# Optimization experiments

Hardware: AMD Instinct MI355X
Metric: run time of the kernel (lower is better)

Reference implementation:

```python
import jax, jax.numpy as jnp
import numpy as np

TOP_K = 2  # config.moe_config['moe_top_k']


def setup_inputs() -> dict:
    key = jax.random.key(0)
    k1, k2, k3, k4 = jax.random.split(key, 4)
    B, S, H, F, E = 2, 1024, 1024, 2048, 8
    def init(k, shape, fan_in):
        return jax.random.normal(k, shape, jnp.float32) / np.float32(np.sqrt(fan_in))
    return {
        "hidden_states": jax.random.normal(k1, (B, S, H), jnp.float32),
        "router_w": init(k2, (H, E), H),          # Linear(hidden, E, bias=False)
        "W1": init(k3, (E, H, 2 * F), H),          # per-expert Linear(hidden, 2*ffn)
        "W2": init(k4, (E, F, H), F),              # per-expert Linear(ffn, hidden)
    }


def reference(hidden_states, router_w, W1, W2):
    B, S, H = hidden_states.shape
    E = router_w.shape[1]
    x = hidden_states.reshape(-1, H)                      # [N, H], N = B*S
    N = x.shape[0]

    # router: logits -> fp32 softmax -> top-k -> renormalize (matches torch)
    logits = x @ router_w                                  # [N, E]
    probs = jax.nn.softmax(logits.astype(jnp.float32), axis=-1)
    rw, sel = jax.lax.top_k(probs, TOP_K)                  # [N, k]
    rw = rw / rw.sum(axis=-1, keepdims=True)
    rw = rw.astype(x.dtype)

    # combine weights per (token, expert); top-k experts are distinct so add==set
    cw = jnp.zeros((N, E), x.dtype).at[jnp.arange(N)[:, None], sel].add(rw)

    # per-expert SwiGLU MLP over all tokens, masked combine (full-capacity MoE)
    h = jnp.einsum('nh,ehf->enf', x, W1)                   # [E, N, 2F]
    a, b = jnp.split(h, 2, axis=-1)                        # gate, value halves
    g = jax.nn.silu(a) * b                                 # [E, N, F]
    y = jnp.einsum('enf,efh->enh', g, W2)                  # [E, N, H]
    out = jnp.einsum('enh,ne->nh', y, cw)                  # weighted scatter-combine
    return out.reshape(B, S, H)
```

## Files before the change

kernel.cpp:

```cpp
#include <hip/hip_runtime.h>
#include <hip/hip_bf16.h>

#define H_DIM 1024
#define E_NUM 8
#define F_DIM 2048
#define N_TOK 2048
typedef unsigned int uint;
typedef short bf16x8 __attribute__((ext_vector_type(8)));
typedef float f32x4 __attribute__((ext_vector_type(4)));

#define WS_CNT   0
#define WS_LIST  256
#define WS_W     (WS_LIST + 8*N_TOK*4)
#define WS_G     131072
#define WS_Y     (WS_G + 4096*2048*2)
#define WS_XB    WS_Y


static __device__ __forceinline__ uint f2bf(float f) {
    uint u = __builtin_bit_cast(uint, f);
    return (u + 0x7FFFu + ((u >> 16) & 1u)) >> 16;
}
static __device__ __forceinline__ float bflo(uint u) { return __builtin_bit_cast(float, u << 16); }
static __device__ __forceinline__ float bfhi(uint u) { return __builtin_bit_cast(float, u & 0xFFFF0000u); }
static __device__ __forceinline__ uint cvtpk(float a, float b) {
    uint r;
    asm("v_cvt_pk_bf16_f32 %0, %1, %2" : "=v"(r) : "v"(a), "v"(b));
    return r;
}
static __device__ __forceinline__ void gload_lds16(const void* g, void* l) {
    __builtin_amdgcn_global_load_lds(
        (const __attribute__((address_space(1))) unsigned int*)g,
        (__attribute__((address_space(3))) unsigned int*)l,
        16, 0, 0);
}
template<int N> static __device__ __forceinline__ void vmwait() {
    if constexpr (N == 0)       asm volatile("s_waitcnt vmcnt(0)" ::: "memory");
    else if constexpr (N == 10) asm volatile("s_waitcnt vmcnt(10)" ::: "memory");
}

__global__ __launch_bounds__(256) void cvt_x_kernel(const float* __restrict__ x,
                                                    unsigned short* __restrict__ xb)
{
    int c = blockIdx.x * 256 + threadIdx.x;
    int row = c >> 7, b = c & 127;
    int t = b >> 3, s = b & 7;
    int klo = t*64 + (s >> 2)*32 + (s & 3)*4;
    const float* xr = x + (size_t)row * H_DIM;
    float4 lo = *(const float4*)(xr + klo);
    float4 hi = *(const float4*)(xr + klo + 16);
    uint4 o;
    o.x = cvtpk(lo.x, lo.y); o.y = cvtpk(lo.z, lo.w);
    o.z = cvtpk(hi.x, hi.y); o.w = cvtpk(hi.z, hi.w);
    *(uint4*)(xb + (size_t)row * H_DIM + b*8) = o;
}

__global__ __launch_bounds__(256) void router_kernel(
    const float* __restrict__ x, const float* __restrict__ rw,
    int* __restrict__ cnt, int* __restrict__ list, float* __restrict__ w_entry)
{
    int wave = threadIdx.x >> 6, lane = threadIdx.x & 63;
    int n = blockIdx.x * 4 + wave;
    const float* xr = x + (size_t)n * H_DIM;
    float acc[8] = {0,0,0,0,0,0,0,0};
    #pragma unroll
    for (int i = 0; i < H_DIM/64; ++i) {
        int h = i*64 + lane;
        float xv = xr[h];
        const float4* rr = (const float4*)(rw + (size_t)h*8);
        float4 r0 = rr[0], r1 = rr[1];
        acc[0] += xv*r0.x; acc[1] += xv*r0.y; acc[2] += xv*r0.z; acc[3] += xv*r0.w;
        acc[4] += xv*r1.x; acc[5] += xv*r1.y; acc[6] += xv*r1.z; acc[7] += xv*r1.w;
    }
    #pragma unroll
    for (int e = 0; e < 8; ++e) {
        float v = acc[e];
        #pragma unroll
        for (int off = 32; off; off >>= 1) v += __shfl_xor(v, off);
        acc[e] = v;
    }
    int e0 = 0;
    #pragma unroll
    for (int e = 1; e < 8; ++e) if (acc[e] > acc[e0]) e0 = e;
    int e1 = -1;
    #pragma unroll
    for (int e = 0; e < 8; ++e) if (e != e0 && (e1 < 0 || acc[e] > acc[e1])) e1 = e;
    float w0 = 1.0f / (1.0f + __expf(acc[e1] - acc[e0]));
    float w1 = 1.0f - w0;
    if (lane == 0) {
        int p0 = atomicAdd(&cnt[e0], 1);
        list[e0*N_TOK + p0] = n*2;
        w_entry[n*2] = w0;
        int p1 = atomicAdd(&cnt[e1], 1);
        list[e1*N_TOK + p1] = n*2 + 1;
        w_entry[n*2+1] = w1;
    }
}

template<int IS_G1>
__global__ __launch_bounds__(256, 2) void moe_gemm_kernel(
    const unsigned short* __restrict__ Asrc, const float* __restrict__ W,
    const int* __restrict__ cnt, const int* __restrict__ list,
    const float* __restrict__ w_entry, unsigned short* __restrict__ dst)
{
    constexpr int KTOT  = IS_G1 ? H_DIM : F_DIM;
    constexpr int BLD   = IS_G1 ? 2*F_DIM : H_DIM;
    constexpr int DLD   = IS_G1 ? F_DIM : H_DIM;
    constexpr int ALD   = IS_G1 ? H_DIM : F_DIM;
    constexpr int NMT   = 32;
    constexpr int NNT   = IS_G1 ? 32 : 8;
    constexpr int NT    = KTOT / 64;

    __shared__ __align__(16) unsigned short As[2][64*64];
    __shared__ __align__(16) uint Bs[2][64*128];

    constexpr int nb = NMT * NNT * E_NUM;
    constexpr int chunk = nb >> 3;
    int bid = blockIdx.x;
    int f  = (bid & 7) * chunk + (bid >> 3);
    int mt = f % NMT;
    int nt = (f / NMT) % NNT;
    int e  = f / (NMT * NNT);

    const int c = cnt[e];
    if (mt * 64 >= c) return;
    const int tid = threadIdx.x;
    const int lane = tid & 63, wid = tid >> 6;
    const int l15 = lane & 15, lg = lane >> 4;
    const int lbase = e * N_TOK + mt * 64;

    const unsigned short* a_src[2];
    #pragma unroll
    for (int i = 0; i < 2; ++i) {
        int sl  = wid*2048 + i*1024 + lane*16;
        int row = sl >> 7;
        int kb  = ((sl >> 4) & 7) ^ (row & 7);
        int rr  = (mt*64 + row) < c ? row : (c - 1 - mt*64);
        int ent = list[lbase + rr];
        int arow = IS_G1 ? (ent >> 1) : ent;
        a_src[i] = Asrc + (size_t)arow * ALD + kb*8;
    }

    const float* Wb = W + (size_t)e * (size_t)(IS_G1 ? H_DIM*2*F_DIM : F_DIM*H_DIM);
    const float* b_srcp[8];
    #pragma unroll
    for (int i = 0; i < 8; ++i) {
        int k  = wid*16 + i*2 + (lane >> 5);
        int c4 = (lane & 31) ^ (k & 12);
        int gc;
        if constexpr (IS_G1) gc = (c4 < 16) ? (nt*64 + 4*c4) : (F_DIM + nt*64 + 4*(c4-16));
        else                 gc = nt*128 + 4*c4;
        b_srcp[i] = Wb + (size_t)k * BLD + gc;
    }

    int a_addr[4][2];
    #pragma unroll
    for (int m = 0; m < 4; ++m)
        #pragma unroll
        for (int kk = 0; kk < 2; ++kk) {
            int row = m*16 + l15;
            a_addr[m][kk] = row*128 + ((kk*64 + lg*16) ^ ((row & 7) << 4));
        }
    int b_base[2];
    #pragma unroll
    for (int j = 0; j < 2; ++j) {
        int cb = j ? (4 + wid) : wid;
        b_base[j] = ((cb*16 + l15) * 4) ^ (lg << 6);
    }

    f32x4 acc[4][2];
    #pragma unroll
    for (int m = 0; m < 4; ++m)
        #pragma unroll
        for (int j = 0; j < 2; ++j) acc[m][j] = (f32x4){0.f,0.f,0.f,0.f};

    auto STAGE = [&](int tt) {
        const int b = tt & 1;
        #pragma unroll
        for (int i = 0; i < 2; ++i)
            gload_lds16(a_src[i] + tt*64, (char*)As[b] + wid*2048 + i*1024);
        #pragma unroll
        for (int i = 0; i < 8; ++i)
            gload_lds16(b_srcp[i] + (size_t)tt * 64 * BLD, (char*)Bs[b] + wid*8192 + i*1024);
    };

    auto compute_step = [&](const char* ab, const char* bb0) {
        #pragma unroll
        for (int kk = 0; kk < 2; ++kk) {
            bf16x8 af[4];
            #pragma unroll
            for (int m = 0; m < 4; ++m)
                af[m] = *(const bf16x8*)(ab + a_addr[m][kk]);
            bf16x8 bfr[2];
            #pragma unroll
            for (int j = 0; j < 2; ++j) {
                const char* bb = bb0 + (kk*32 + 4*lg)*512 + b_base[j];
                float fA0 = *(const float*)(bb);
                float fA1 = *(const float*)(bb + 512);
                float fA2 = *(const float*)(bb + 1024);
                float fA3 = *(const float*)(bb + 1536);
                float fB0 = *(const float*)(bb + 8192);
                float fB1 = *(const float*)(bb + 8192 + 512);
                float fB2 = *(const float*)(bb + 8192 + 1024);
                float fB3 = *(const float*)(bb + 8192 + 1536);
                union { uint u[4]; bf16x8 v; } bu;
                bu.u[0] = cvtpk(fA0, fA1);
                bu.u[1] = cvtpk(fA2, fA3);
                bu.u[2] = cvtpk(fB0, fB1);
                bu.u[3] = cvtpk(fB2, fB3);
                bfr[j] = bu.v;
            }
            #pragma unroll
            for (int m = 0; m < 4; ++m)
                #pragma unroll
                for (int j = 0; j < 2; ++j)
                    acc[m][j] = __builtin_amdgcn_mfma_f32_16x16x32_bf16(af[m], bfr[j], acc[m][j], 0, 0, 0);
        }
    };

    STAGE(0);
    STAGE(1);

    #pragma unroll
    for (int t = 0; t < NT; ++t) {
        if (t < NT - 1) vmwait<10>();
        else            vmwait<0>();
        __builtin_amdgcn_sched_barrier(0);
        __builtin_amdgcn_s_barrier();
        asm volatile("" ::: "memory");
        compute_step((const char*)As[t & 1], (const char*)Bs[t & 1]);
        if (t + 2 < NT) {
            asm volatile("" ::: "memory");
            __builtin_amdgcn_s_barrier();
            asm volatile("" ::: "memory");
            STAGE(t + 2);
        }
    }

    if constexpr (IS_G1) {
        const int pbase = nt*64 + ((wid >> 1)*4 + (l15 >> 2))*8 + (wid & 1)*4 + (l15 & 3);
        #pragma unroll
        for (int m = 0; m < 4; ++m) {
            f32x4 ga = acc[m][0], gv = acc[m][1];
            #pragma unroll
            for (int i = 0; i < 4; ++i) {
                int rl = m*16 + lg*4 + i;
                if (mt*64 + rl < c) {
                    int ent = list[lbase + rl];
                    float a = ga[i];
                    float g = (a / (1.f + __expf(-a))) * gv[i];
                    dst[(size_t)ent * DLD + pbase] = (unsigned short)f2bf(g);
                }
            }
        }
    } else {
        #pragma unroll
        for (int m = 0; m < 4; ++m)
            #pragma unroll
            for (int i = 0; i < 4; ++i) {
                int rl = m*16 + lg*4 + i;
                if (mt*64 + rl < c) {
                    int ent = list[lbase + rl];
                    float w = w_entry[ent];
                    #pragma unroll
                    for (int j = 0; j < 2; ++j) {
                        int col = nt*128 + (j ? (64 + wid*16) : (wid*16)) + l15;
                        dst[(size_t)ent * DLD + col] = (unsigned short)f2bf(w * acc[m][j][i]);
                    }
                }
            }
    }
}

__global__ __launch_bounds__(256) void combine_kernel(
    const unsigned short* __restrict__ y, float* __restrict__ out)
{
    int gid = blockIdx.x * 256 + threadIdx.x;
    size_t base = (size_t)gid * 8;
    int n = (int)(base >> 10), h = (int)(base & 1023);
    const uint4 a = *(const uint4*)(y + (size_t)(2*n)   * 1024 + h);
    const uint4 b = *(const uint4*)(y + (size_t)(2*n+1) * 1024 + h);
    float4 o0, o1;
    o0.x = bflo(a.x)+bflo(b.x); o0.y = bfhi(a.x)+bfhi(b.x);
    o0.z = bflo(a.y)+bflo(b.y); o0.w = bfhi(a.y)+bfhi(b.y);
    o1.x = bflo(a.z)+bflo(b.z); o1.y = bfhi(a.z)+bfhi(b.z);
    o1.z = bflo(a.w)+bflo(b.w); o1.w = bfhi(a.w)+bfhi(b.w);
    *(float4*)(out + base)     = o0;
    *(float4*)(out + base + 4) = o1;
}

extern "C" void kernel_launch(void* const* d_in, const int* in_sizes, int n_in,
                              void* d_out, int out_size, void* d_ws, size_t ws_size,
                              hipStream_t stream) {
    const float* x  = (const float*)d_in[0];
    const float* rw = (const float*)d_in[1];
    const float* W1 = (const float*)d_in[2];
    const float* W2 = (const float*)d_in[3];
    float* out = (float*)d_out;
    char* ws = (char*)d_ws;
    int*   cnt     = (int*)(ws + WS_CNT);
    int*   list    = (int*)(ws + WS_LIST);
    float* w_entry = (float*)(ws + WS_W);
    unsigned short* g  = (unsigned short*)(ws + WS_G);
    unsigned short* y  = (unsigned short*)(ws + WS_Y);
    unsigned short* xb = (unsigned short*)(ws + WS_XB);

    hipMemsetAsync(cnt, 0, E_NUM * sizeof(int), stream);
    cvt_x_kernel<<<N_TOK*H_DIM/2048, 256, 0, stream>>>(x, xb);
    router_kernel<<<N_TOK/4, 256, 0, stream>>>(x, rw, cnt, list, w_entry);
    moe_gemm_kernel<1><<<32*32*E_NUM, 256, 0, stream>>>(xb, W1, cnt, list, w_entry, g);
    moe_gemm_kernel<0><<<32*8*E_NUM, 256, 0, stream>>>(g,  W2, cnt, list, w_entry, y);
    combine_kernel<<<(out_size/8 + 255)/256, 256, 0, stream>>>(y, out);
}
```

Before: 254.2 us.

## Shrink K-step and GEMM2 row tile, raise occupancy, stage epilogue through LDS

The K step of the grouped GEMM pipeline drops from 64 to 32 so each B buffer is half the size. The A tile is staged once per two B stages. GEMM2 now uses 32-row tiles with twice as many blocks, and launch bounds ask for 3 or 4 blocks per CU instead of 2, which should improve occupancy and latency hiding. Both epilogues now transpose results through shared memory so each thread writes 16- or 32-byte vectors per gathered row instead of scattered 2-byte stores. In exchange there are more barriers per K, and GEMM2 blocks do less work each, so the W2 tile is re-read more often.

Result: faster. 237.4 us (-6.6%).

```diff
diff --git a/kernel.cpp b/kernel.cpp
--- a/kernel.cpp
+++ b/kernel.cpp
@@ -35,8 +35,10 @@
         16, 0, 0);
 }
 template<int N> static __device__ __forceinline__ void vmwait() {
-    if constexpr (N == 0)       asm volatile("s_waitcnt vmcnt(0)" ::: "memory");
-    else if constexpr (N == 10) asm volatile("s_waitcnt vmcnt(10)" ::: "memory");
+    if constexpr (N == 0)      asm volatile("s_waitcnt vmcnt(0)" ::: "memory");
+    else if constexpr (N == 4) asm volatile("s_waitcnt vmcnt(4)" ::: "memory");
+    else if constexpr (N == 5) asm volatile("s_waitcnt vmcnt(5)" ::: "memory");
+    else if constexpr (N == 6) asm volatile("s_waitcnt vmcnt(6)" ::: "memory");
 }
 
 __global__ __launch_bounds__(256) void cvt_x_kernel(const float* __restrict__ x,
@@ -98,7 +100,7 @@
 }
 
 template<int IS_G1>
-__global__ __launch_bounds__(256, 2) void moe_gemm_kernel(
+__global__ __launch_bounds__(256, IS_G1 ? 3 : 4) void moe_gemm_kernel(
     const unsigned short* __restrict__ Asrc, const float* __restrict__ W,
     const int* __restrict__ cnt, const int* __restrict__ list,
     const float* __restrict__ w_entry, unsigned short* __restrict__ dst)
@@ -107,12 +109,16 @@
     constexpr int BLD   = IS_G1 ? 2*F_DIM : H_DIM;
     constexpr int DLD   = IS_G1 ? F_DIM : H_DIM;
     constexpr int ALD   = IS_G1 ? H_DIM : F_DIM;
-    constexpr int NMT   = 32;
+    constexpr int ROWS  = IS_G1 ? 64 : 32;
+    constexpr int NM    = ROWS / 16;
+    constexpr int NA    = ROWS / 32;
+    constexpr int NMT   = 2048 / ROWS;
     constexpr int NNT   = IS_G1 ? 32 : 8;
-    constexpr int NT    = KTOT / 64;
-
-    __shared__ __align__(16) unsigned short As[2][64*64];
-    __shared__ __align__(16) uint Bs[2][64*128];
+    constexpr int NT    = KTOT / 32;
+    constexpr int ODDW  = 4 + NA;
+
+    __shared__ __align__(16) unsigned short As[2][ROWS*64];
+    __shared__ __align__(16) uint Bs[2][32*128];
 
     constexpr int nb = NMT * NNT * E_NUM;
     constexpr int chunk = nb >> 3;
@@ -123,29 +129,29 @@
     int e  = f / (NMT * NNT);
 
     const int c = cnt[e];
-    if (mt * 64 >= c) return;
+    if (mt * ROWS >= c) return;
     const int tid = threadIdx.x;
     const int lane = tid & 63, wid = tid >> 6;
     const int l15 = lane & 15, lg = lane >> 4;
-    const int lbase = e * N_TOK + mt * 64;
-
-    const unsigned short* a_src[2];
-    #pragma unroll
-    for (int i = 0; i < 2; ++i) {
-        int sl  = wid*2048 + i*1024 + lane*16;
+    const int lbase = e * N_TOK + mt * ROWS;
+
+    const unsigned short* a_src[NA];
+    #pragma unroll
+    for (int i = 0; i < NA; ++i) {
+        int sl  = wid*(NA*1024) + i*1024 + lane*16;
         int row = sl >> 7;
         int kb  = ((sl >> 4) & 7) ^ (row & 7);
-        int rr  = (mt*64 + row) < c ? row : (c - 1 - mt*64);
+        int rr  = (mt*ROWS + row) < c ? row : (c - 1 - mt*ROWS);
         int ent = list[lbase + rr];
         int arow = IS_G1 ? (ent >> 1) : ent;
         a_src[i] = Asrc + (size_t)arow * ALD + kb*8;
     }
 
     const float* Wb = W + (size_t)e * (size_t)(IS_G1 ? H_DIM*2*F_DIM : F_DIM*H_DIM);
-    const float* b_srcp[8];
-    #pragma unroll
-    for (int i = 0; i < 8; ++i) {
-        int k  = wid*16 + i*2 + (lane >> 5);
+    const float* b_srcp[4];
+    #pragma unroll
+    for (int i = 0; i < 4; ++i) {
+        int k  = wid*8 + i*2 + (lane >> 5);
         int c4 = (lane & 31) ^ (k & 12);
         int gc;
         if constexpr (IS_G1) gc = (c4 < 16) ? (nt*64 + 4*c4) : (F_DIM + nt*64 + 4*(c4-16));
@@ -153,122 +159,159 @@
         b_srcp[i] = Wb + (size_t)k * BLD + gc;
     }
 
-    int a_addr[4][2];
-    #pragma unroll
-    for (int m = 0; m < 4; ++m)
-        #pragma unroll
-        for (int kk = 0; kk < 2; ++kk) {
+    int a_addr[NM][2];
+    #pragma unroll
+    for (int m = 0; m < NM; ++m)
+        #pragma unroll
+        for (int p = 0; p < 2; ++p) {
             int row = m*16 + l15;
-            a_addr[m][kk] = row*128 + ((kk*64 + lg*16) ^ ((row & 7) << 4));
+            a_addr[m][p] = row*128 + ((p*64 + lg*16) ^ ((row & 7) << 4));
         }
     int b_base[2];
     #pragma unroll
     for (int j = 0; j < 2; ++j) {
-        int cb = j ? (4 + wid) : wid;
+        int cb = IS_G1 ? (j ? (4 + wid) : wid) : (wid*2 + j);
         b_base[j] = ((cb*16 + l15) * 4) ^ (lg << 6);
     }
 
-    f32x4 acc[4][2];
-    #pragma unroll
-    for (int m = 0; m < 4; ++m)
+    f32x4 acc[NM][2];
+    #pragma unroll
+    for (int m = 0; m < NM; ++m)
         #pragma unroll
         for (int j = 0; j < 2; ++j) acc[m][j] = (f32x4){0.f,0.f,0.f,0.f};
 
-    auto STAGE = [&](int tt) {
-        const int b = tt & 1;
-        #pragma unroll
-        for (int i = 0; i < 2; ++i)
-            gload_lds16(a_src[i] + tt*64, (char*)As[b] + wid*2048 + i*1024);
-        #pragma unroll
-        for (int i = 0; i < 8; ++i)
-            gload_lds16(b_srcp[i] + (size_t)tt * 64 * BLD, (char*)Bs[b] + wid*8192 + i*1024);
+    auto STAGE_A = [&](int s) {
+        #pragma unroll
+        for (int i = 0; i < NA; ++i)
+            gload_lds16(a_src[i] + s*64, (char*)As[s & 1] + wid*(NA*1024) + i*1024);
     };
-
-    auto compute_step = [&](const char* ab, const char* bb0) {
-        #pragma unroll
-        for (int kk = 0; kk < 2; ++kk) {
-            bf16x8 af[4];
+    auto STAGE_B = [&](int t) {
+        #pragma unroll
+        for (int i = 0; i < 4; ++i)
+            gload_lds16(b_srcp[i] + (size_t)t * 32 * BLD, (char*)Bs[t & 1] + wid*4096 + i*1024);
+    };
+    auto compute = [&](int P, int abuf) {
+        const char* ab  = (const char*)As[abuf];
+        const char* bb0 = (const char*)Bs[P];
+        bf16x8 af[NM];
+        #pragma unroll
+        for (int m = 0; m < NM; ++m)
+            af[m] = *(const bf16x8*)(ab + (P ? a_addr[m][1] : a_addr[m][0]));
+        bf16x8 bfr[2];
+        #pragma unroll
+        for (int j = 0; j < 2; ++j) {
+            const char* bb = bb0 + (4*lg)*512 + b_base[j];
+            float fA0 = *(const float*)(bb);
+            float fA1 = *(const float*)(bb + 512);
+            float fA2 = *(const float*)(bb + 1024);
+            float fA3 = *(const float*)(bb + 1536);
+            float fB0 = *(const float*)(bb + 8192);
+            float fB1 = *(const float*)(bb + 8192 + 512);
+            float fB2 = *(const float*)(bb + 8192 + 1024);
+            float fB3 = *(const float*)(bb + 8192 + 1536);
+            union { uint u[4]; bf16x8 v; } bu;
+            bu.u[0] = cvtpk(fA0, fA1);
+            bu.u[1] = cvtpk(fA2, fA3);
+            bu.u[2] = cvtpk(fB0, fB1);
+            bu.u[3] = cvtpk(fB2, fB3);
+            bfr[j] = bu.v;
+        }
+        #pragma unroll
+        for (int m = 0; m < NM; ++m)
             #pragma unroll
-            for (int m = 0; m < 4; ++m)
-                af[m] = *(const bf16x8*)(ab + a_addr[m][kk]);
-            bf16x8 bfr[2];
-            #pragma unroll
-            for (int j = 0; j < 2; ++j) {
-                const char* bb = bb0 + (kk*32 + 4*lg)*512 + b_base[j];
-                float fA0 = *(const float*)(bb);
-                float fA1 = *(const float*)(bb + 512);
-                float fA2 = *(const float*)(bb + 1024);
-                float fA3 = *(const float*)(bb + 1536);
-                float fB0 = *(const float*)(bb + 8192);
-                float fB1 = *(const float*)(bb + 8192 + 512);
-                float fB2 = *(const float*)(bb + 8192 + 1024);
-                float fB3 = *(const float*)(bb + 8192 + 1536);
-                union { uint u[4]; bf16x8 v; } bu;
-                bu.u[0] = cvtpk(fA0, fA1);
-                bu.u[1] = cvtpk(fA2, fA3);
-                bu.u[2] = cvtpk(fB0, fB1);
-                bu.u[3] = cvtpk(fB2, fB3);
-                bfr[j] = bu.v;
-            }
-            #pragma unroll
-            for (int m = 0; m < 4; ++m)
-                #pragma unroll
-                for (int j = 0; j < 2; ++j)
-                    acc[m][j] = __builtin_amdgcn_mfma_f32_16x16x32_bf16(af[m], bfr[j], acc[m][j], 0, 0, 0);
-        }
+            for (int j = 0; j < 2; ++j)
+                acc[m][j] = __builtin_amdgcn_mfma_f32_16x16x32_bf16(af[m], bfr[j], acc[m][j], 0, 0, 0);
     };
 
-    STAGE(0);
-    STAGE(1);
-
-    #pragma unroll
-    for (int t = 0; t < NT; ++t) {
-        if (t < NT - 1) vmwait<10>();
-        else            vmwait<0>();
+    STAGE_A(0); STAGE_B(0); STAGE_B(1);
+
+    for (int tp = 0; tp < NT/2 - 1; ++tp) {
+        const int t = 2*tp, ab = tp & 1;
+        vmwait<4>();
         __builtin_amdgcn_sched_barrier(0);
         __builtin_amdgcn_s_barrier();
         asm volatile("" ::: "memory");
-        compute_step((const char*)As[t & 1], (const char*)Bs[t & 1]);
-        if (t + 2 < NT) {
-            asm volatile("" ::: "memory");
-            __builtin_amdgcn_s_barrier();
-            asm volatile("" ::: "memory");
-            STAGE(t + 2);
-        }
+        compute(0, ab);
+        asm volatile("" ::: "memory");
+        __builtin_amdgcn_s_barrier();
+        asm volatile("" ::: "memory");
+        STAGE_A(tp + 1);
+        STAGE_B(t + 2);
+        vmwait<ODDW>();
+        __builtin_amdgcn_sched_barrier(0);
+        __builtin_amdgcn_s_barrier();
+        asm volatile("" ::: "memory");
+        compute(1, ab);
+        asm volatile("" ::: "memory");
+        __builtin_amdgcn_s_barrier();
+        asm volatile("" ::: "memory");
+        STAGE_B(t + 3);
+    }
+    {
+        const int ab = (NT/2 - 1) & 1;
+        vmwait<4>();
+        __builtin_amdgcn_sched_barrier(0);
+        __builtin_amdgcn_s_barrier();
+        asm volatile("" ::: "memory");
+        compute(0, ab);
+        asm volatile("" ::: "memory");
+        vmwait<0>();
+        __builtin_amdgcn_sched_barrier(0);
+        __builtin_amdgcn_s_barrier();
+        asm volatile("" ::: "memory");
+        compute(1, ab);
     }
 
     if constexpr (IS_G1) {
-        const int pbase = nt*64 + ((wid >> 1)*4 + (l15 >> 2))*8 + (wid & 1)*4 + (l15 & 3);
-        #pragma unroll
-        for (int m = 0; m < 4; ++m) {
+        unsigned short (*tb)[64] = (unsigned short (*)[64])As;
+        const int pcol = ((wid >> 1)*4 + (l15 >> 2))*8 + (wid & 1)*4 + (l15 & 3);
+        #pragma unroll
+        for (int m = 0; m < NM; ++m) {
             f32x4 ga = acc[m][0], gv = acc[m][1];
             #pragma unroll
             for (int i = 0; i < 4; ++i) {
-                int rl = m*16 + lg*4 + i;
-                if (mt*64 + rl < c) {
-                    int ent = list[lbase + rl];
-                    float a = ga[i];
-                    float g = (a / (1.f + __expf(-a))) * gv[i];
-                    dst[(size_t)ent * DLD + pbase] = (unsigned short)f2bf(g);
+                int row = m*16 + lg*4 + i;
+                float a = ga[i];
+                tb[row][pcol] = (unsigned short)f2bf((a / (1.f + __expf(-a))) * gv[i]);
+            }
+        }
+        __syncthreads();
+        int r = tid >> 3, ch = tid & 7;
+        #pragma unroll
+        for (int h = 0; h < 2; ++h) {
+            int rr = r + h*32;
+            if (mt*64 + rr < c) {
+                int ent = list[lbase + rr];
+                uint4 v = *(const uint4*)&tb[rr][ch*8];
+                *(uint4*)((char*)dst + ((size_t)ent * DLD + nt*64)*2 + ch*16) = v;
+            }
+        }
+    } else {
+        float (*tb)[128] = (float (*)[128])Bs;
+        #pragma unroll
+        for (int m = 0; m < NM; ++m)
+            #pragma unroll
+            for (int j = 0; j < 2; ++j)
+                #pragma unroll
+                for (int i = 0; i < 4; ++i) {
+                    int row = m*16 + lg*4 + i;
+                    tb[row][(wid*2 + j)*16 + l15] = acc[m][j][i];
                 }
-            }
-        }
-    } else {
-        #pragma unroll
-        for (int m = 0; m < 4; ++m)
-            #pragma unroll
-            for (int i = 0; i < 4; ++i) {
-                int rl = m*16 + lg*4 + i;
-                if (mt*64 + rl < c) {
-                    int ent = list[lbase + rl];
-                    float w = w_entry[ent];
-                    #pragma unroll
-                    for (int j = 0; j < 2; ++j) {
-                        int col = nt*128 + (j ? (64 + wid*16) : (wid*16)) + l15;
-                        dst[(size_t)ent * DLD + col] = (unsigned short)f2bf(w * acc[m][j][i]);
-                    }
-                }
-            }
+        __syncthreads();
+        int r = tid >> 3, ch = tid & 7;
+        if (mt*32 + r < c) {
+            int ent = list[lbase + r];
+            float w = w_entry[ent];
+            const float* src = &tb[r][ch*16];
+            uint4 o0, o1;
+            o0.x = cvtpk(w*src[0],  w*src[1]);  o0.y = cvtpk(w*src[2],  w*src[3]);
+            o0.z = cvtpk(w*src[4],  w*src[5]);  o0.w = cvtpk(w*src[6],  w*src[7]);
+            o1.x = cvtpk(w*src[8],  w*src[9]);  o1.y = cvtpk(w*src[10], w*src[11]);
+            o1.z = cvtpk(w*src[12], w*src[13]); o1.w = cvtpk(w*src[14], w*src[15]);
+            char* dp = (char*)dst + ((size_t)ent * DLD + nt*128 + ch*16)*2;
+            *(uint4*)(dp)      = o0;
+            *(uint4*)(dp + 16) = o1;
+        }
     }
 }
 
@@ -309,6 +352,6 @@
     cvt_x_kernel<<<N_TOK*H_DIM/2048, 256, 0, stream>>>(x, xb);
     router_kernel<<<N_TOK/4, 256, 0, stream>>>(x, rw, cnt, list, w_entry);
     moe_gemm_kernel<1><<<32*32*E_NUM, 256, 0, stream>>>(xb, W1, cnt, list, w_entry, g);
-    moe_gemm_kernel<0><<<32*8*E_NUM, 256, 0, stream>>>(g,  W2, cnt, list, w_entry, y);
+    moe_gemm_kernel<0><<<64*8*E_NUM, 256, 0, stream>>>(g,  W2, cnt, list, w_entry, y);
     combine_kernel<<<(out_size/8 + 255)/256, 256, 0, stream>>>(y, out);
 }
```
